# Kernel tuning notes

Measured on AMD Instinct MI355X. Metric: run time of the kernel, lower is better.

The kernel has to match this reference:

```python
import jax, jax.numpy as jnp
import numpy as np

NUM_POINTS = 17  # number of t quadrature points
T_MAX = 2.0
VAR_GAMMA = 1.0
B, D, K = 8192, 2048, 512


def setup_inputs() -> dict:
    key = jax.random.key(0)
    k1, k2 = jax.random.split(key)
    embeddings = jax.random.normal(k1, (B, D), dtype=jnp.float32)
    directions = jax.random.normal(k2, (D, K), dtype=jnp.float32)
    return {"embeddings": embeddings, "directions": directions}


def reference(embeddings, directions):
    z = embeddings.astype(jnp.float32)

    # VICReg-style variance floor on raw embedding dims (unbiased std, as torch)
    cls_std = jnp.std(z, axis=0, ddof=1)
    var_floor = jnp.mean(jax.nn.relu(VAR_GAMMA - cls_std))

    # F.normalize(directions, dim=0): divide by column L2 norm (clamped at 1e-12)
    norms = jnp.maximum(jnp.linalg.norm(directions, axis=0, keepdims=True), 1e-12)
    d = directions / norms

    proj = z @ d  # (B, K)
    std = jnp.std(proj, axis=0, ddof=1)
    proj = (proj - jnp.mean(proj, axis=0, keepdims=True)) / (std + 1e-8)

    # Trapezoid quadrature over t in (0, T_MAX]
    t = jnp.linspace(0.0, T_MAX, NUM_POINTS + 1)[1:]          # (T,)
    dt = T_MAX / NUM_POINTS
    w = jnp.full((NUM_POINTS,), dt).at[0].set(dt / 2).at[-1].set(dt / 2)

    # All t-points in one fused pass: (T, B, K)
    tp = t[:, None, None] * proj[None, :, :]
    ecf_real = jnp.mean(jnp.cos(tp), axis=1)                  # (T, K)
    ecf_imag = jnp.mean(jnp.sin(tp), axis=1)                  # (T, K)
    tcf = jnp.exp(-0.5 * t * t)[:, None]                      # (T, 1) target CF N(0,1)

    integrand = ecf_real ** 2 + ecf_imag ** 2 - 2.0 * ecf_real * tcf + tcf ** 2
    total = jnp.sum(w * jnp.mean(integrand, axis=1))
    return total + var_floor
```

## Files before the change

kernel.cpp:

```cpp
#include <hip/hip_runtime.h>
#include <hip/hip_bf16.h>

#define BB   8192
#define DD   2048
#define KK   512
#define TT   17

#define BM   128
#define BN   128
#define BK   128
#define NT   (DD / BK)

#define NZB  512

typedef __attribute__((ext_vector_type(8))) short  bf16x8;
typedef __attribute__((ext_vector_type(4))) float  f32x4;

__device__ __forceinline__ void gload16(const void* g, void* l) {
  __builtin_amdgcn_global_load_lds(
      (const __attribute__((address_space(1))) void*)g,
      (__attribute__((address_space(3))) void*)l,
      16, 0, 0);
}

__global__ __launch_bounds__(256) void prep_z_kernel(
    const float* __restrict__ z, unsigned short* __restrict__ zb,
    float* __restrict__ part2) {
  int c = threadIdx.x * 8;
  int r0 = blockIdx.x * 16;
  float s[8] = {0,0,0,0,0,0,0,0}, ss[8] = {0,0,0,0,0,0,0,0};
  for (int ch = 0; ch < 4; ++ch) {
    float4 u[4][2];
    #pragma unroll
    for (int rr = 0; rr < 4; ++rr) {
      const float* p = &z[(size_t)(r0 + ch * 4 + rr) * DD + c];
      u[rr][0] = *(const float4*)p;
      u[rr][1] = *(const float4*)(p + 4);
    }
    #pragma unroll
    for (int rr = 0; rr < 4; ++rr) {
      float f[8] = {u[rr][0].x, u[rr][0].y, u[rr][0].z, u[rr][0].w,
                    u[rr][1].x, u[rr][1].y, u[rr][1].z, u[rr][1].w};
      bf16x8 o;
      #pragma unroll
      for (int i = 0; i < 8; ++i) {
        s[i] += f[i]; ss[i] += f[i] * f[i];
        __hip_bfloat16 h = __float2bfloat16(f[i]);
        o[i] = *(short*)&h;
      }
      *(bf16x8*)&zb[(size_t)(r0 + ch * 4 + rr) * DD + c] = o;
    }
  }
  float* pb = part2 + (size_t)blockIdx.x * 4096;
  *(float4*)&pb[c]        = (float4){s[0], s[1], s[2], s[3]};
  *(float4*)&pb[c + 4]    = (float4){s[4], s[5], s[6], s[7]};
  *(float4*)&pb[2048 + c]     = (float4){ss[0], ss[1], ss[2], ss[3]};
  *(float4*)&pb[2048 + c + 4] = (float4){ss[4], ss[5], ss[6], ss[7]};
}

__global__ __launch_bounds__(256) void reduce2_kernel(
    const float* __restrict__ part2, float* __restrict__ part5,
    const float* __restrict__ dir, float* __restrict__ part3) {
  int bid = blockIdx.x;
  int tid = threadIdx.x;
  if (bid < 256) {
    int dgrp = bid & 63, bq = bid >> 6;
    int d = dgrp * 64 + (tid & 63);
    int ch = tid >> 6;
    int b0 = bq * 128 + ch * 32;
    float s = 0.f;
    for (int b = b0; b < b0 + 32; ++b)
      s += part2[(size_t)b * 4096 + d];
    __shared__ float rs[4][64];
    rs[ch][tid & 63] = s;
    __syncthreads();
    if (tid < 64)
      part5[(size_t)bq * 4096 + dgrp * 64 + tid] =
          rs[0][tid] + rs[1][tid] + rs[2][tid] + rs[3][tid];
  } else {
    int rg = bid - 256;
    int c4 = tid & 127;
    int half = tid >> 7;
    int r0 = rg * 64 + half;
    float4 q = {0.f, 0.f, 0.f, 0.f};
    #pragma unroll 8
    for (int i = 0; i < 32; ++i) {
      float4 v = *(const float4*)&dir[(size_t)(r0 + 2 * i) * KK + c4 * 4];
      q.x += v.x * v.x; q.y += v.y * v.y; q.z += v.z * v.z; q.w += v.w * v.w;
    }
    __shared__ float rd[2][512];
    *(float4*)&rd[half][c4 * 4] = q;
    __syncthreads();
    if (tid < 128) {
      float4 a = *(float4*)&rd[0][tid * 4];
      float4 b = *(float4*)&rd[1][tid * 4];
      float4 o = {a.x + b.x, a.y + b.y, a.z + b.z, a.w + b.w};
      *(float4*)&part3[(size_t)rg * KK + tid * 4] = o;
    }
  }
}

__global__ __launch_bounds__(256) void finalize1_kernel(
    const float* __restrict__ part5, const float* __restrict__ part3,
    float* __restrict__ invnorm, float* __restrict__ out,
    float* __restrict__ psum) {
  int tid = threadIdx.x;
  for (int i = tid; i < 2 * KK; i += 256) psum[i] = 0.f;
  for (int k = tid; k < KK; k += 256) {
    float ssq = 0.f;
    #pragma unroll
    for (int i = 0; i < 32; ++i) ssq += part3[(size_t)i * KK + k];
    float n = sqrtf(ssq);
    invnorm[k] = 1.0f / fmaxf(n, 1e-12f);
  }
  float acc = 0.f;
  for (int d = tid; d < DD; d += 256) {
    float s = 0.f, ss = 0.f;
    #pragma unroll
    for (int i = 0; i < 4; ++i) {
      s  += part5[i * 4096 + d];
      ss += part5[i * 4096 + 2048 + d];
    }
    float var = (ss - s * s / (float)BB) / (float)(BB - 1);
    float sd = sqrtf(fmaxf(var, 0.f));
    acc += fmaxf(1.0f - sd, 0.0f);
  }
  __shared__ float red[256];
  red[tid] = acc; __syncthreads();
  for (int s = 128; s > 0; s >>= 1) {
    if (tid < s) red[tid] += red[tid + s];
    __syncthreads();
  }
  if (tid == 0) out[0] = red[0] / (float)DD;
}

__global__ __launch_bounds__(256) void dirT_kernel(
    const float* __restrict__ dir, const float* __restrict__ invnorm,
    unsigned short* __restrict__ dT) {
  __shared__ unsigned short tile[64][65];
  int n0 = blockIdx.x * 64;
  int d0 = blockIdx.y * 64;
  int tx = threadIdx.x & 63, ty = threadIdx.x >> 6;
  float inv = invnorm[n0 + tx];
  #pragma unroll
  for (int i = 0; i < 16; ++i) {
    int dr = ty + i * 4;
    float v = dir[(size_t)(d0 + dr) * KK + n0 + tx] * inv;
    __hip_bfloat16 h = __float2bfloat16(v);
    tile[dr][tx] = *(unsigned short*)&h;
  }
  __syncthreads();
  #pragma unroll
  for (int i = 0; i < 16; ++i) {
    int nr = ty + i * 4;
    dT[(size_t)(n0 + nr) * DD + d0 + tx] = tile[tx][nr];
  }
}

__global__ __launch_bounds__(256) void gemm_bf16_kernel(
    const unsigned short* __restrict__ zb, const unsigned short* __restrict__ dT,
    float* __restrict__ proj, float* __restrict__ psum, float* __restrict__ psumsq) {
  __shared__ __align__(16) short As[2][BM * BK];
  __shared__ __align__(16) short Bs[2][BN * BK];

  int tid = threadIdx.x;
  int w = tid >> 6, l = tid & 63;

  int bid = blockIdx.x;
  int xcd = bid & 7, slot = bid >> 3;
  int bmi = xcd * 8 + (slot >> 2);
  int bni = slot & 3;
  int bm = bmi * BM, bn = bni * BN;

  int r4 = l >> 4;
  int gsw_e = ((l & 15) ^ r4) * 8;
  int gsw_o = ((l & 15) ^ (r4 + 4)) * 8;
  const unsigned short* aRow = zb + (size_t)(bm + w * 32 + r4) * DD;
  const unsigned short* bRow = dT + (size_t)(bn + w * 32 + r4) * DD;

#define STAGE(buf, kt) do {                                                   \
    const unsigned short* a_ = aRow + (size_t)(kt) * BK;                      \
    const unsigned short* b_ = bRow + (size_t)(kt) * BK;                      \
    gload16(a_ + 0 * 4 * DD + gsw_e, &As[buf][(w * 32 + 0) * BK]);            \
    gload16(b_ + 0 * 4 * DD + gsw_e, &Bs[buf][(w * 32 + 0) * BK]);            \
    gload16(a_ + 1 * 4 * DD + gsw_o, &As[buf][(w * 32 + 4) * BK]);            \
    gload16(b_ + 1 * 4 * DD + gsw_o, &Bs[buf][(w * 32 + 4) * BK]);            \
    gload16(a_ + 2 * 4 * DD + gsw_e, &As[buf][(w * 32 + 8) * BK]);            \
    gload16(b_ + 2 * 4 * DD + gsw_e, &Bs[buf][(w * 32 + 8) * BK]);            \
    gload16(a_ + 3 * 4 * DD + gsw_o, &As[buf][(w * 32 + 12) * BK]);           \
    gload16(b_ + 3 * 4 * DD + gsw_o, &Bs[buf][(w * 32 + 12) * BK]);           \
    gload16(a_ + 4 * 4 * DD + gsw_e, &As[buf][(w * 32 + 16) * BK]);           \
    gload16(b_ + 4 * 4 * DD + gsw_e, &Bs[buf][(w * 32 + 16) * BK]);           \
    gload16(a_ + 5 * 4 * DD + gsw_o, &As[buf][(w * 32 + 20) * BK]);           \
    gload16(b_ + 5 * 4 * DD + gsw_o, &Bs[buf][(w * 32 + 20) * BK]);           \
    gload16(a_ + 6 * 4 * DD + gsw_e, &As[buf][(w * 32 + 24) * BK]);           \
    gload16(b_ + 6 * 4 * DD + gsw_e, &Bs[buf][(w * 32 + 24) * BK]);           \
    gload16(a_ + 7 * 4 * DD + gsw_o, &As[buf][(w * 32 + 28) * BK]);           \
    gload16(b_ + 7 * 4 * DD + gsw_o, &Bs[buf][(w * 32 + 28) * BK]);           \
  } while (0)

  int wm = (w >> 1) * 64, wn = (w & 1) * 64;
  int fr = l & 15, fq = l >> 4;
  int fx = fr & 7;

  f32x4 acc[4][4];
  f32x4 zero4 = {0.f, 0.f, 0.f, 0.f};
  #pragma unroll
  for (int mi = 0; mi < 4; ++mi)
    #pragma unroll
    for (int ni = 0; ni < 4; ++ni) acc[mi][ni] = zero4;

  STAGE(0, 0);
  asm volatile("s_waitcnt vmcnt(0)" ::: "memory");
  __builtin_amdgcn_s_barrier();

  for (int t = 0; t < NT; ++t) {
    int cur = t & 1;
    if (t + 1 < NT) STAGE(cur ^ 1, t + 1);
    #pragma unroll
    for (int kk = 0; kk < 4; ++kk) {
      bf16x8 av[4], bv[4];
      int go = ((kk * 4 + fq) ^ fx) * 8;
      #pragma unroll
      for (int mi = 0; mi < 4; ++mi)
        av[mi] = *(const bf16x8*)&As[cur][(wm + mi * 16 + fr) * BK + go];
      #pragma unroll
      for (int ni = 0; ni < 4; ++ni)
        bv[ni] = *(const bf16x8*)&Bs[cur][(wn + ni * 16 + fr) * BK + go];
      #pragma unroll
      for (int mi = 0; mi < 4; ++mi)
        #pragma unroll
        for (int ni = 0; ni < 4; ++ni)
          acc[mi][ni] = __builtin_amdgcn_mfma_f32_16x16x32_bf16(av[mi], bv[ni], acc[mi][ni], 0, 0, 0);
    }
    asm volatile("s_waitcnt vmcnt(0)" ::: "memory");
    __builtin_amdgcn_s_barrier();
  }
#undef STAGE

  #pragma unroll
  for (int ni = 0; ni < 4; ++ni) {
    float s = 0.f, q = 0.f;
    int col = bn + wn + ni * 16 + fr;
    #pragma unroll
    for (int mi = 0; mi < 4; ++mi)
      #pragma unroll
      for (int j = 0; j < 4; ++j) {
        float v = acc[mi][ni][j];
        s += v; q += v * v;
        proj[(size_t)(bm + wm + mi * 16 + fq * 4 + j) * KK + col] = v;
      }
    s += __shfl_xor(s, 16); q += __shfl_xor(q, 16);
    s += __shfl_xor(s, 32); q += __shfl_xor(q, 32);
    if (fq == 0) {
      atomicAdd(&psum[col], s);
      atomicAdd(&psumsq[col], q);
    }
  }
}

__global__ __launch_bounds__(256) void ecf_kernel(
    const float* __restrict__ proj, const float* __restrict__ psum,
    const float* __restrict__ psumsq, float* __restrict__ part) {
  int kx = blockIdx.x, ry = blockIdx.y;
  int tid = threadIdx.x;
  int kl = tid & 63, w = tid >> 6;
  int k = kx * 64 + kl;
  float sk = psum[k], qk = psumsq[k];
  float m = sk / (float)BB;
  float var = (qk - sk * sk / (float)BB) / (float)(BB - 1);
  float sd = sqrtf(fmaxf(var, 0.f));
  float is = 1.0f / (sd + 1e-8f);
  int r0 = ry * 128 + w * 32;
  const float dt = 2.0f / 17.0f;

  float ac[TT], as[TT];
  #pragma unroll
  for (int j = 0; j < TT; ++j) { ac[j] = 0.f; as[j] = 0.f; }

  #pragma unroll 4
  for (int i = 0; i < 32; ++i) {
    float p = (proj[(size_t)(r0 + i) * KK + k] - m) * is;
    float th = dt * p;
    float s1, c1;
    __sincosf(th, &s1, &c1);
    float tc = 2.0f * c1;
    float cj = c1, sj = s1, cjm = 1.0f, sjm = 0.0f;
    ac[0] += c1; as[0] += s1;
    #pragma unroll
    for (int j = 1; j < TT; ++j) {
      float cn = tc * cj - cjm;
      float sn = tc * sj - sjm;
      cjm = cj; sjm = sj; cj = cn; sj = sn;
      ac[j] += cj; as[j] += sj;
    }
  }

  __shared__ float red[4 * 2176];
  int base = w * 2176 + kl * 34;
  #pragma unroll
  for (int j = 0; j < TT; ++j) {
    red[base + j] = ac[j];
    red[base + 17 + j] = as[j];
  }
  __syncthreads();
  for (int idx = tid; idx < 2176; idx += 256) {
    float v = red[idx] + red[2176 + idx] + red[4352 + idx] + red[6528 + idx];
    part[(size_t)(ry * 8 + kx) * 2176 + idx] = v;
  }
}

__global__ __launch_bounds__(256) void ecf_final_kernel(
    const float* __restrict__ part, float* __restrict__ out) {
  int gi = blockIdx.x * 256 + threadIdx.x;
  int kx = gi / 1088;
  int r2 = gi - kx * 1088;
  int kl = r2 / 17;
  int j  = r2 - kl * 17;
  const float dt = 2.0f / 17.0f;
  float cs = 0.f, ss = 0.f;
  for (int ry = 0; ry < 64; ++ry) {
    size_t b = (size_t)(ry * 8 + kx) * 2176 + kl * 34;
    cs += part[b + j];
    ss += part[b + 17 + j];
  }
  const float invB = 1.0f / (float)BB;
  float r  = cs * invB;
  float im = ss * invB;
  float t = dt * (float)(j + 1);
  float wq = (j == 0 || j == TT - 1) ? dt * 0.5f : dt;
  float tcf = expf(-0.5f * t * t);
  float val = wq * (r * r + im * im - 2.0f * r * tcf + tcf * tcf) / (float)KK;

  __shared__ float red[256];
  int tid = threadIdx.x;
  red[tid] = val; __syncthreads();
  for (int s = 128; s > 0; s >>= 1) {
    if (tid < s) red[tid] += red[tid + s];
    __syncthreads();
  }
  if (tid == 0) atomicAdd(out, red[0]);
}

extern "C" void kernel_launch(void* const* d_in, const int* in_sizes, int n_in,
                              void* d_out, int out_size, void* d_ws, size_t ws_size,
                              hipStream_t stream) {
  const float* z   = (const float*)d_in[0];
  const float* dir = (const float*)d_in[1];
  float* out = (float*)d_out;

  uint8_t* w8 = (uint8_t*)d_ws;
  unsigned short* zb = (unsigned short*)w8;
  float* part        = (float*)w8;
  unsigned short* dT = (unsigned short*)(w8 + 33554432);
  float* proj        = (float*)(w8 + 35651584);
  float* part2       = (float*)(w8 + 35651584);
  float* stat        = (float*)(w8 + 52428800);
  float* part5    = stat;
  float* psum     = part5 + 16384;
  float* psumsq   = psum + KK;
  float* invnorm  = psumsq + KK;
  float* part3    = invnorm + KK;

  prep_z_kernel<<<dim3(NZB), 256, 0, stream>>>(z, zb, part2);
  reduce2_kernel<<<dim3(288), 256, 0, stream>>>(part2, part5, dir, part3);
  finalize1_kernel<<<1, 256, 0, stream>>>(part5, part3, invnorm, out, psum);
  dirT_kernel<<<dim3(8, 32), 256, 0, stream>>>(dir, invnorm, dT);
  gemm_bf16_kernel<<<dim3(256), 256, 0, stream>>>(zb, dT, proj, psum, psumsq);
  ecf_kernel<<<dim3(8, 64), 256, 0, stream>>>(proj, psum, psumsq, part);
  ecf_final_kernel<<<dim3(34), 256, 0, stream>>>(part, out);
}
```

Baseline: 102.3 us.

## Fuse finalize into dirT kernel and store projections as bf16

```diff
diff --git a/kernel.cpp b/kernel.cpp
--- a/kernel.cpp
+++ b/kernel.cpp
@@ -100,66 +100,72 @@
   }
 }
 
-__global__ __launch_bounds__(256) void finalize1_kernel(
-    const float* __restrict__ part5, const float* __restrict__ part3,
-    float* __restrict__ invnorm, float* __restrict__ out,
-    float* __restrict__ psum) {
-  int tid = threadIdx.x;
-  for (int i = tid; i < 2 * KK; i += 256) psum[i] = 0.f;
-  for (int k = tid; k < KK; k += 256) {
+__global__ __launch_bounds__(256) void dirT_kernel(
+    const float* __restrict__ dir, const float* __restrict__ part3,
+    const float* __restrict__ part5, unsigned short* __restrict__ dT,
+    float* __restrict__ out, float* __restrict__ psum) {
+  int bid = blockIdx.x;
+  int tid = threadIdx.x;
+  if (bid < 256) {
+    __shared__ unsigned short tile[64][65];
+    __shared__ float fold[4][64];
+    __shared__ float sinv[64];
+    int n0 = (bid & 7) * 64;
+    int d0 = (bid >> 3) * 64;
+    int tx = tid & 63, ty = tid >> 6;
     float ssq = 0.f;
     #pragma unroll
-    for (int i = 0; i < 32; ++i) ssq += part3[(size_t)i * KK + k];
-    float n = sqrtf(ssq);
-    invnorm[k] = 1.0f / fmaxf(n, 1e-12f);
-  }
-  float acc = 0.f;
-  for (int d = tid; d < DD; d += 256) {
-    float s = 0.f, ss = 0.f;
-    #pragma unroll
-    for (int i = 0; i < 4; ++i) {
-      s  += part5[i * 4096 + d];
-      ss += part5[i * 4096 + 2048 + d];
-    }
-    float var = (ss - s * s / (float)BB) / (float)(BB - 1);
-    float sd = sqrtf(fmaxf(var, 0.f));
-    acc += fmaxf(1.0f - sd, 0.0f);
-  }
-  __shared__ float red[256];
-  red[tid] = acc; __syncthreads();
-  for (int s = 128; s > 0; s >>= 1) {
-    if (tid < s) red[tid] += red[tid + s];
-    __syncthreads();
-  }
-  if (tid == 0) out[0] = red[0] / (float)DD;
-}
-
-__global__ __launch_bounds__(256) void dirT_kernel(
-    const float* __restrict__ dir, const float* __restrict__ invnorm,
-    unsigned short* __restrict__ dT) {
-  __shared__ unsigned short tile[64][65];
-  int n0 = blockIdx.x * 64;
-  int d0 = blockIdx.y * 64;
-  int tx = threadIdx.x & 63, ty = threadIdx.x >> 6;
-  float inv = invnorm[n0 + tx];
-  #pragma unroll
-  for (int i = 0; i < 16; ++i) {
-    int dr = ty + i * 4;
-    float v = dir[(size_t)(d0 + dr) * KK + n0 + tx] * inv;
-    __hip_bfloat16 h = __float2bfloat16(v);
-    tile[dr][tx] = *(unsigned short*)&h;
-  }
-  __syncthreads();
-  #pragma unroll
-  for (int i = 0; i < 16; ++i) {
-    int nr = ty + i * 4;
-    dT[(size_t)(n0 + nr) * DD + d0 + tx] = tile[tx][nr];
+    for (int i = 0; i < 8; ++i)
+      ssq += part3[(size_t)(ty * 8 + i) * KK + n0 + tx];
+    fold[ty][tx] = ssq;
+    __syncthreads();
+    if (tid < 64) {
+      float t = fold[0][tid] + fold[1][tid] + fold[2][tid] + fold[3][tid];
+      sinv[tid] = 1.0f / fmaxf(sqrtf(t), 1e-12f);
+    }
+    __syncthreads();
+    float inv = sinv[tx];
+    #pragma unroll
+    for (int i = 0; i < 16; ++i) {
+      int dr = ty + i * 4;
+      float v = dir[(size_t)(d0 + dr) * KK + n0 + tx] * inv;
+      __hip_bfloat16 h = __float2bfloat16(v);
+      tile[dr][tx] = *(unsigned short*)&h;
+    }
+    __syncthreads();
+    #pragma unroll
+    for (int i = 0; i < 16; ++i) {
+      int nr = ty + i * 4;
+      dT[(size_t)(n0 + nr) * DD + d0 + tx] = tile[tx][nr];
+    }
+  } else {
+    for (int i = tid; i < 2 * KK; i += 256) psum[i] = 0.f;
+    float acc = 0.f;
+    for (int d = tid; d < DD; d += 256) {
+      float s = 0.f, ss = 0.f;
+      #pragma unroll
+      for (int i = 0; i < 4; ++i) {
+        s  += part5[i * 4096 + d];
+        ss += part5[i * 4096 + 2048 + d];
+      }
+      float var = (ss - s * s / (float)BB) / (float)(BB - 1);
+      float sd = sqrtf(fmaxf(var, 0.f));
+      acc += fmaxf(1.0f - sd, 0.0f);
+    }
+    __shared__ float red[256];
+    red[tid] = acc; __syncthreads();
+    for (int s = 128; s > 0; s >>= 1) {
+      if (tid < s) red[tid] += red[tid + s];
+      __syncthreads();
+    }
+    if (tid == 0) out[0] = red[0] / (float)DD;
   }
 }
 
 __global__ __launch_bounds__(256) void gemm_bf16_kernel(
     const unsigned short* __restrict__ zb, const unsigned short* __restrict__ dT,
-    float* __restrict__ proj, float* __restrict__ psum, float* __restrict__ psumsq) {
+    unsigned short* __restrict__ projb, float* __restrict__ psum,
+    float* __restrict__ psumsq) {
   __shared__ __align__(16) short As[2][BM * BK];
   __shared__ __align__(16) short Bs[2][BN * BK];
 
@@ -248,7 +254,9 @@
       for (int j = 0; j < 4; ++j) {
         float v = acc[mi][ni][j];
         s += v; q += v * v;
-        proj[(size_t)(bm + wm + mi * 16 + fq * 4 + j) * KK + col] = v;
+        __hip_bfloat16 h = __float2bfloat16(v);
+        projb[(size_t)(bm + wm + mi * 16 + fq * 4 + j) * KK + col] =
+            *(unsigned short*)&h;
       }
     s += __shfl_xor(s, 16); q += __shfl_xor(q, 16);
     s += __shfl_xor(s, 32); q += __shfl_xor(q, 32);
@@ -260,7 +268,7 @@
 }
 
 __global__ __launch_bounds__(256) void ecf_kernel(
-    const float* __restrict__ proj, const float* __restrict__ psum,
+    const unsigned short* __restrict__ projb, const float* __restrict__ psum,
     const float* __restrict__ psumsq, float* __restrict__ part) {
   int kx = blockIdx.x, ry = blockIdx.y;
   int tid = threadIdx.x;
@@ -280,7 +288,9 @@
 
   #pragma unroll 4
   for (int i = 0; i < 32; ++i) {
-    float p = (proj[(size_t)(r0 + i) * KK + k] - m) * is;
+    unsigned short u = projb[(size_t)(r0 + i) * KK + k];
+    float pv = __bfloat162float(*(const __hip_bfloat16*)&u);
+    float p = (pv - m) * is;
     float th = dt * p;
     float s1, c1;
     __sincosf(th, &s1, &c1);
@@ -350,23 +360,21 @@
   float* out = (float*)d_out;
 
   uint8_t* w8 = (uint8_t*)d_ws;
-  unsigned short* zb = (unsigned short*)w8;
-  float* part        = (float*)w8;
-  unsigned short* dT = (unsigned short*)(w8 + 33554432);
-  float* proj        = (float*)(w8 + 35651584);
-  float* part2       = (float*)(w8 + 35651584);
-  float* stat        = (float*)(w8 + 52428800);
+  unsigned short* zb    = (unsigned short*)w8;
+  float* part           = (float*)w8;
+  unsigned short* dT    = (unsigned short*)(w8 + 33554432);
+  unsigned short* projb = (unsigned short*)(w8 + 35651584);
+  float* part2          = (float*)(w8 + 35651584);
+  float* stat           = (float*)(w8 + 52428800);
   float* part5    = stat;
   float* psum     = part5 + 16384;
   float* psumsq   = psum + KK;
-  float* invnorm  = psumsq + KK;
-  float* part3    = invnorm + KK;
+  float* part3    = psumsq + KK;
 
   prep_z_kernel<<<dim3(NZB), 256, 0, stream>>>(z, zb, part2);
   reduce2_kernel<<<dim3(288), 256, 0, stream>>>(part2, part5, dir, part3);
-  finalize1_kernel<<<1, 256, 0, stream>>>(part5, part3, invnorm, out, psum);
-  dirT_kernel<<<dim3(8, 32), 256, 0, stream>>>(dir, invnorm, dT);
-  gemm_bf16_kernel<<<dim3(256), 256, 0, stream>>>(zb, dT, proj, psum, psumsq);
-  ecf_kernel<<<dim3(8, 64), 256, 0, stream>>>(proj, psum, psumsq, part);
+  dirT_kernel<<<dim3(257), 256, 0, stream>>>(dir, part3, part5, dT, out, psum);
+  gemm_bf16_kernel<<<dim3(256), 256, 0, stream>>>(zb, dT, projb, psum, psumsq);
+  ecf_kernel<<<dim3(8, 64), 256, 0, stream>>>(projb, psum, psumsq, part);
   ecf_final_kernel<<<dim3(34), 256, 0, stream>>>(part, out);
 }
```

Measured after the change: 94.91 us (median of 2 runs). -7.2%, faster.
